# Kernel tuning notes

Hardware: AMD Instinct MI355X
Metric: run time of the kernel (lower is better)

The kernel has to match this reference:

```python
import jax, jax.numpy as jnp
import numpy as np

VOL_DIM = 256  # stored volume is [256,256,256,1]


def _deform(c, W1, b1, W2, b2, W3, b3, Wf, bf):
    # chain of 1x1x1 convs (== per-voxel matmuls) with cos activations, residual *5
    h = jnp.cos(jnp.einsum('...c,cd->...d', c, W1) + b1)
    h = jnp.cos(jnp.einsum('...c,cd->...d', h, W2) + b2)
    h = jnp.cos(jnp.einsum('...c,cd->...d', h, W3) + b3)
    return c + 5.0 * (jnp.einsum('...c,cd->...d', h, Wf) + bf)


def _trilinear_sample(vol, coords):
    # vol: [X,Y,Z,C]; coords: [...,3] in voxel units (identity nifti edges)
    X, Y, Z, _ = vol.shape
    hi = jnp.array([X - 1, Y - 1, Z - 1], dtype=coords.dtype)
    c = jnp.clip(coords, 0.0, hi)
    c0 = jnp.floor(c)
    f = c - c0
    i0 = c0.astype(jnp.int32)
    i1 = jnp.minimum(i0 + 1, jnp.array([X - 1, Y - 1, Z - 1], jnp.int32))
    x0, y0, z0 = i0[..., 0], i0[..., 1], i0[..., 2]
    x1, y1, z1 = i1[..., 0], i1[..., 1], i1[..., 2]
    fx, fy, fz = f[..., 0:1], f[..., 1:2], f[..., 2:3]
    gx, gy, gz = 1.0 - fx, 1.0 - fy, 1.0 - fz
    out = (vol[x0, y0, z0] * (gx * gy * gz) + vol[x1, y0, z0] * (fx * gy * gz)
         + vol[x0, y1, z0] * (gx * fy * gz) + vol[x0, y0, z1] * (gx * gy * fz)
         + vol[x1, y1, z0] * (fx * fy * gz) + vol[x1, y0, z1] * (fx * gy * fz)
         + vol[x0, y1, z1] * (gx * fy * fz) + vol[x1, y1, z1] * (fx * fy * fz))
    return out  # [...,C]


def setup_inputs() -> dict:
    key = jax.random.key(0)
    ks = jax.random.split(key, 12)
    B, P = 64, 32
    # coords in [0, 255] world==voxel units; extra intensity channel (unused by call)
    coords = jax.random.uniform(ks[0], (B, P, P, P, 3), jnp.float32) * (VOL_DIM - 1.0)
    inten = jax.random.normal(ks[1], (B, P, P, P, 1), jnp.float32)
    x = jnp.concatenate([coords, inten], axis=-1)
    s = 0.1
    return {
        'x': x,
        'W1': jax.random.normal(ks[2], (3, 32), jnp.float32) * s,
        'b1': jax.random.normal(ks[3], (32,), jnp.float32) * s,
        'W2': jax.random.normal(ks[4], (32, 32), jnp.float32) * s,
        'b2': jax.random.normal(ks[5], (32,), jnp.float32) * s,
        'W3': jax.random.normal(ks[6], (32, 32), jnp.float32) * s,
        'b3': jax.random.normal(ks[7], (32,), jnp.float32) * s,
        'Wf': jax.random.normal(ks[8], (32, 3), jnp.float32) * s,
        'bf': jax.random.normal(ks[9], (3,), jnp.float32) * s,
        'vol': jax.random.normal(ks[10], (VOL_DIM, VOL_DIM, VOL_DIM, 1), jnp.float32),
    }


def reference(x, W1, b1, W2, b2, W3, b3, Wf, bf, vol):
    c = x[..., 0:3]                                   # world coords
    c = _deform(c, W1, b1, W2, b2, W3, b3, Wf, bf)    # deformed coords
    return _trilinear_sample(vol, c)                  # [B,32,32,32,1]
```

## Files before the change

kernel.cpp:

```cpp
#include <hip/hip_runtime.h>


#define NPTS (64 * 32 * 32 * 32)
#define NBLK (NPTS / 256)
#define SSTR 40

#define BXN 86
#define BYN 128
#define BZN 86
#define NBRICK (BXN * BYN * BZN)
#define RETILE_T (NBRICK * 8)
#define RETILE_BLK (RETILE_T / 256)

typedef __attribute__((ext_vector_type(8))) short bf16x8;
typedef __attribute__((ext_vector_type(4))) short s16x4;
typedef __attribute__((ext_vector_type(4))) float f32x4;
typedef unsigned long long u64;
typedef unsigned short u16;

__device__ __forceinline__ short bf16rne(float f) {
    unsigned u = __builtin_bit_cast(unsigned, f);
    return (short)((u + 0x7fffu + ((u >> 16) & 1u)) >> 16);
}
__device__ __forceinline__ float bf16tof(short s) {
    return __builtin_bit_cast(float, ((unsigned)(unsigned short)s) << 16);
}
__device__ __forceinline__ float h2f(u16 h) {
    return (float)__builtin_bit_cast(_Float16, h);
}
__device__ __forceinline__ u16 f2h(float f) {
    return __builtin_bit_cast(u16, (_Float16)f);
}

__global__ __launch_bounds__(256)
void retile_k(const float4* __restrict__ vol, u64* __restrict__ dst) {
    int t   = blockIdx.x * 256 + threadIdx.x;
    int q   = t & 7;
    int gz  = (t >> 3) & 63;
    int gyx = t >> 9;
    int x = ((gyx >> 7) << 2) + (q >> 1);
    int y = ((gyx & 127) << 1) + (q & 1);
    float4 v = vol[(((x << 8) + y) << 6) + gz];
    u64 r =  (u64)f2h(v.x)
          | ((u64)f2h(v.y) << 16)
          | ((u64)f2h(v.z) << 32)
          | ((u64)f2h(v.w) << 48);
    dst[t] = r;
}

__global__ __launch_bounds__(256)
void retile_halo_k(const float* __restrict__ vol, u64* __restrict__ dst) {
    int t  = blockIdx.x * 256 + threadIdx.x;
    int q  = t & 7;
    int b  = t >> 3;
    int bz = (int)((unsigned)b % 86u);
    int r  = (int)((unsigned)b / 86u);
    int by = r & 127;
    int bx = r >> 7;
    int x  = min(bx * 3 + (q >> 1), 255);
    int y  = (by << 1) + (q & 1);
    int z0 = bz * 3;
    const float* row = vol + (((x << 8) + y) << 8);
    float v0 = row[z0];
    float v1 = row[min(z0 + 1, 255)];
    float v2 = row[min(z0 + 2, 255)];
    float v3 = row[min(z0 + 3, 255)];
    u64 rr = (u64)f2h(v0)
          | ((u64)f2h(v1) << 16)
          | ((u64)f2h(v2) << 32)
          | ((u64)f2h(v3) << 48);
    dst[t] = rr;
}

template <int MODE>
__global__ __launch_bounds__(256, 8)
void deform_sample_k(const float4* __restrict__ x,
                     const float4* __restrict__ W1,
                     const float4* __restrict__ b1,
                     const float*  __restrict__ W2,
                     const float*  __restrict__ b2,
                     const float*  __restrict__ W3,
                     const float*  __restrict__ b3,
                     const float*  __restrict__ Wf,
                     const float*  __restrict__ bf_,
                     const float*  __restrict__ volf,
                     const u64*    __restrict__ volh,
                     float* __restrict__ out)
{
    __shared__ short lds[4 * 64 * SSTR];
    const int tid  = threadIdx.x;
    const int lane = tid & 63;
    const int wv   = tid >> 6;
    const int m16  = lane & 15;
    const int q    = lane >> 4;
    short* __restrict__ L = &lds[wv * 64 * SSTR];

    const int p = blockIdx.x * 256 + tid;

    const float4 xv = x[p];
    const float c0 = xv.x, c1 = xv.y, c2 = xv.z;

    {
        bf16x8 hw;
        #pragma unroll
        for (int j4 = 0; j4 < 8; ++j4) {
            float4 wa = W1[j4], wb = W1[8 + j4], wc = W1[16 + j4], bb = b1[j4];
            float v0 = __cosf(fmaf(c0, wa.x, fmaf(c1, wb.x, fmaf(c2, wc.x, bb.x))));
            float v1 = __cosf(fmaf(c0, wa.y, fmaf(c1, wb.y, fmaf(c2, wc.y, bb.y))));
            float v2 = __cosf(fmaf(c0, wa.z, fmaf(c1, wb.z, fmaf(c2, wc.z, bb.z))));
            float v3 = __cosf(fmaf(c0, wa.w, fmaf(c1, wb.w, fmaf(c2, wc.w, bb.w))));
            int o = (j4 & 1) * 4;
            hw[o+0] = bf16rne(v0); hw[o+1] = bf16rne(v1);
            hw[o+2] = bf16rne(v2); hw[o+3] = bf16rne(v3);
            if (j4 & 1)
                *(bf16x8*)&L[lane * SSTR + (j4 - 1) * 4] = hw;
        }
    }
    __syncthreads();

    const float* const Wly[2] = { W2, W3 };
    const float* const bly[2] = { b2, b3 };
    #pragma unroll
    for (int ly = 0; ly < 2; ++ly) {
        const float* __restrict__ W  = Wly[ly];
        const float* __restrict__ bb = bly[ly];
        bf16x8 A0, A1;
        #pragma unroll
        for (int j = 0; j < 8; ++j) {
            A0[j] = bf16rne(W[(q * 8 + j) * 32 + m16]);
            A1[j] = bf16rne(W[(q * 8 + j) * 32 + 16 + m16]);
        }
        const float4 blo = *(const float4*)&bb[q * 4];
        const float4 bhi = *(const float4*)&bb[16 + q * 4];

        #pragma unroll
        for (int t = 0; t < 4; ++t) {
            bf16x8 bfrag = *(const bf16x8*)&L[(t * 16 + m16) * SSTR + q * 8];
            f32x4 z = { 0.f, 0.f, 0.f, 0.f };
            f32x4 d0 = __builtin_amdgcn_mfma_f32_16x16x32_bf16(A0, bfrag, z, 0, 0, 0);
            f32x4 d1 = __builtin_amdgcn_mfma_f32_16x16x32_bf16(A1, bfrag, z, 0, 0, 0);

            s16x4 w0, w1;
            w0[0] = bf16rne(__cosf(d0[0] + blo.x));
            w0[1] = bf16rne(__cosf(d0[1] + blo.y));
            w0[2] = bf16rne(__cosf(d0[2] + blo.z));
            w0[3] = bf16rne(__cosf(d0[3] + blo.w));
            w1[0] = bf16rne(__cosf(d1[0] + bhi.x));
            w1[1] = bf16rne(__cosf(d1[1] + bhi.y));
            w1[2] = bf16rne(__cosf(d1[2] + bhi.z));
            w1[3] = bf16rne(__cosf(d1[3] + bhi.w));
            *(s16x4*)&L[(t * 16 + m16) * SSTR + q * 4]      = w0;
            *(s16x4*)&L[(t * 16 + m16) * SSTR + 16 + q * 4] = w1;
        }
        __syncthreads();
    }

    float d0 = bf_[0], d1 = bf_[1], d2 = bf_[2];
    #pragma unroll
    for (int j4 = 0; j4 < 8; ++j4) {
        s16x4 v = *(const s16x4*)&L[lane * SSTR + j4 * 4];
        #pragma unroll
        for (int r = 0; r < 4; ++r) {
            float hv = bf16tof(v[r]);
            int ii = j4 * 4 + r;
            d0 = fmaf(hv, Wf[3*ii+0], d0);
            d1 = fmaf(hv, Wf[3*ii+1], d1);
            d2 = fmaf(hv, Wf[3*ii+2], d2);
        }
    }
    float e0 = fmaf(5.f, d0, c0);
    float e1 = fmaf(5.f, d1, c1);
    float e2 = fmaf(5.f, d2, c2);

    e0 = fminf(fmaxf(e0, 0.f), 255.f);
    e1 = fminf(fmaxf(e1, 0.f), 255.f);
    e2 = fminf(fmaxf(e2, 0.f), 255.f);
    float fl0 = floorf(e0), fl1 = floorf(e1), fl2 = floorf(e2);
    float fx = e0 - fl0, fy = e1 - fl1, fz = e2 - fl2;
    float gx = 1.f - fx, gy = 1.f - fy, gz = 1.f - fz;
    int x0 = (int)fl0, y0 = (int)fl1, z0 = (int)fl2;
    int x1 = min(x0 + 1, 255), y1 = min(y0 + 1, 255), z1 = min(z0 + 1, 255);

    float v000, v001, v010, v011, v100, v101, v110, v111;

    if constexpr (MODE == 2) {
        int bx = (int)((unsigned)x0 / 3u);  int lx = x0 - bx * 3;
        int by = y0 >> 1;                   int ly = y0 & 1;
        int bz = (int)((unsigned)z0 / 3u);  int lz = z0 - bz * 3;
        const char* vb = (const char*)volh;
        const int lineA = ((((bx << 7) + by) * 86) + bz) << 6;
        const int byB   = min(by + 1, 127);
        const int lineB = (ly == 0) ? lineA
                                    : (((((bx << 7) + byB) * 86) + bz) << 6);
        const int yrowB = (ly == 0) ? 1 : ((y0 == 255) ? 1 : 0);
        const int offA  = lx * 16 + ly * 8;
        const int offB  = lx * 16 + yrowB * 8;
        u64 LA0 = *(const u64*)(vb + lineA + offA);
        u64 LA1 = *(const u64*)(vb + lineA + offA + 16);
        u64 LB0 = *(const u64*)(vb + lineB + offB);
        u64 LB1 = *(const u64*)(vb + lineB + offB + 16);
        const int sh = lz * 16;
        u64 sA0 = LA0 >> sh, sA1 = LA1 >> sh, sB0 = LB0 >> sh, sB1 = LB1 >> sh;
        v000 = h2f((u16)sA0);  v001 = h2f((u16)(sA0 >> 16));
        v100 = h2f((u16)sA1);  v101 = h2f((u16)(sA1 >> 16));
        v010 = h2f((u16)sB0);  v011 = h2f((u16)(sB0 >> 16));
        v110 = h2f((u16)sB1);  v111 = h2f((u16)(sB1 >> 16));
    } else if constexpr (MODE == 1) {
        const int lz  = z0 & 3;
        const int zp  = (z0 >> 2) << 6;
        const int xp0 = ((x0 >> 2) << 19) | ((x0 & 3) << 4);
        const int xp1 = ((x1 >> 2) << 19) | ((x1 & 3) << 4);
        const int yp0 = ((y0 >> 1) << 12) | ((y0 & 1) << 3);
        const int yp1 = ((y1 >> 1) << 12) | ((y1 & 1) << 3);
        const char* vb = (const char*)volh;
        const int a00 = xp0 | yp0 | zp, a10 = xp1 | yp0 | zp;
        const int a01 = xp0 | yp1 | zp, a11 = xp1 | yp1 | zp;
        u64 L00 = *(const u64*)(vb + a00);
        u64 L10 = *(const u64*)(vb + a10);
        u64 L01 = *(const u64*)(vb + a01);
        u64 L11 = *(const u64*)(vb + a11);
        u64 H00 = 0, H10 = 0, H01 = 0, H11 = 0;
        const bool crossz = (lz == 3) && (z0 < 255);
        if (crossz) {
            H00 = *(const u64*)(vb + a00 + 64);
            H10 = *(const u64*)(vb + a10 + 64);
            H01 = *(const u64*)(vb + a01 + 64);
            H11 = *(const u64*)(vb + a11 + 64);
        }
        const int sh = lz * 16;
        const bool in_line = (lz < 3);
        auto ext = [&](u64 lo, u64 hi, float& a, float& b) {
            u64 s = lo >> sh;
            a = h2f((u16)s);
            float b_in = h2f((u16)(s >> 16));
            float b_nx = h2f((u16)hi);
            b = in_line ? b_in : (crossz ? b_nx : a);
        };
        ext(L00, H00, v000, v001);
        ext(L10, H10, v100, v101);
        ext(L01, H01, v010, v011);
        ext(L11, H11, v110, v111);
    } else {
        int b00 = (x0 << 16) | (y0 << 8);
        int b01 = (x0 << 16) | (y1 << 8);
        int b10 = (x1 << 16) | (y0 << 8);
        int b11 = (x1 << 16) | (y1 << 8);
        v000 = volf[b00 + z0]; v001 = volf[b00 + z1];
        v010 = volf[b01 + z0]; v011 = volf[b01 + z1];
        v100 = volf[b10 + z0]; v101 = volf[b10 + z1];
        v110 = volf[b11 + z0]; v111 = volf[b11 + z1];
    }

    float r = gz * (gy * (gx*v000 + fx*v100) + fy * (gx*v010 + fx*v110))
            + fz * (gy * (gx*v001 + fx*v101) + fy * (gx*v011 + fx*v111));

    out[p] = r;
}

extern "C" void kernel_launch(void* const* d_in, const int* in_sizes, int n_in,
                              void* d_out, int out_size, void* d_ws, size_t ws_size,
                              hipStream_t stream) {
    const float4* x   = (const float4*)d_in[0];
    const float4* W1  = (const float4*)d_in[1];
    const float4* b1  = (const float4*)d_in[2];
    const float*  W2  = (const float*)d_in[3];
    const float*  b2  = (const float*)d_in[4];
    const float*  W3  = (const float*)d_in[5];
    const float*  b3  = (const float*)d_in[6];
    const float*  Wf  = (const float*)d_in[7];
    const float*  bf_ = (const float*)d_in[8];
    const float*  vol = (const float*)d_in[9];
    float* out = (float*)d_out;

    const size_t needH = (size_t)NBRICK * 64;
    const size_t need1 = (size_t)4194304 * 8;
    if (ws_size >= needH) {
        u64* volh = (u64*)d_ws;
        retile_halo_k<<<RETILE_BLK, 256, 0, stream>>>(vol, volh);
        deform_sample_k<2><<<NBLK, 256, 0, stream>>>(x, W1, b1, W2, b2, W3, b3,
                                                     Wf, bf_, nullptr, volh, out);
    } else if (ws_size >= need1) {
        u64* volh = (u64*)d_ws;
        retile_k<<<16384, 256, 0, stream>>>((const float4*)vol, volh);
        deform_sample_k<1><<<NBLK, 256, 0, stream>>>(x, W1, b1, W2, b2, W3, b3,
                                                     Wf, bf_, nullptr, volh, out);
    } else {
        deform_sample_k<0><<<NBLK, 256, 0, stream>>>(x, W1, b1, W2, b2, W3, b3,
                                                     Wf, bf_, vol, nullptr, out);
    }
}
```

Before: 213.4 us.

## Add full y-halo fp16 brick layout so each sample reads one contiguous line

Adds a new retile kernel that builds one brick per y row with a y+1 halo (3 x-slices by 2 y-rows by 4 z), doubling the staged volume footprint, plus a new sampling mode that fetches all 8 corners as four consecutive u64 loads from a single 64-byte brick. The goal is to remove the second-line fetch and the branchy offset logic of the previous halo layout, which loaded from two bricks when y was odd. In exchange the retile writes about twice as many bytes and needs a larger workspace; if the workspace is too small the code falls back to the old path.

```diff
diff --git a/kernel.cpp b/kernel.cpp
--- a/kernel.cpp
+++ b/kernel.cpp
@@ -11,10 +11,17 @@
 #define NBRICK (BXN * BYN * BZN)
 #define RETILE_T (NBRICK * 8)
 #define RETILE_BLK (RETILE_T / 256)
+#define HALO_BYTES ((size_t)NBRICK * 64)
+
+#define NBRICK_F (86 * 256 * 86)
+#define RETILE2_T (NBRICK_F * 4)
+#define RETILE2_BLK (RETILE2_T / 256)
+#define FULL_BYTES ((size_t)NBRICK_F * 64)
 
 typedef __attribute__((ext_vector_type(8))) short bf16x8;
 typedef __attribute__((ext_vector_type(4))) short s16x4;
 typedef __attribute__((ext_vector_type(4))) float f32x4;
+typedef __attribute__((ext_vector_type(2))) unsigned long long u64x2;
 typedef unsigned long long u64;
 typedef unsigned short u16;
 
@@ -72,6 +79,36 @@
     dst[t] = rr;
 }
 
+__global__ __launch_bounds__(256)
+void retile_full2_k(const float* __restrict__ vol, u64* __restrict__ dst) {
+    int t  = blockIdx.x * 256 + threadIdx.x;
+    int dx = t & 3;
+    int b  = t >> 2;
+    int bz = (int)((unsigned)b % 86u);
+    int r  = (int)((unsigned)b / 86u);
+    int by = r & 255;
+    int bx = r >> 8;
+    int x  = min(bx * 3 + dx, 255);
+    int y1 = min(by + 1, 255);
+    int z0 = bz * 3;
+    int zl = (z0 > 252) ? 252 : z0;
+    const float* row0 = vol + (((x << 8) + by) << 8) + zl;
+    const float* row1 = vol + (((x << 8) + y1) << 8) + zl;
+    float va[4], vb[4];
+    __builtin_memcpy(va, row0, 16);
+    __builtin_memcpy(vb, row1, 16);
+    if (z0 == 255) {
+        va[0] = va[1] = va[2] = va[3];
+        vb[0] = vb[1] = vb[2] = vb[3];
+    }
+    u64 lo = (u64)f2h(va[0]) | ((u64)f2h(va[1]) << 16)
+           | ((u64)f2h(va[2]) << 32) | ((u64)f2h(va[3]) << 48);
+    u64 hi = (u64)f2h(vb[0]) | ((u64)f2h(vb[1]) << 16)
+           | ((u64)f2h(vb[2]) << 32) | ((u64)f2h(vb[3]) << 48);
+    u64x2 st; st.x = lo; st.y = hi;
+    *(u64x2*)(dst + (b << 3) + (dx << 1)) = st;
+}
+
 template <int MODE>
 __global__ __launch_bounds__(256, 8)
 void deform_sample_k(const float4* __restrict__ x,
@@ -183,7 +220,21 @@
 
     float v000, v001, v010, v011, v100, v101, v110, v111;
 
-    if constexpr (MODE == 2) {
+    if constexpr (MODE == 3) {
+        int bx = (int)((unsigned)x0 / 3u);  int lx = x0 - bx * 3;
+        int bz = (int)((unsigned)z0 / 3u);  int lz = z0 - bz * 3;
+        const u64* g = volh + ((((bx << 8) + y0) * 86 + bz) << 3) + (lx << 1);
+        u64 g0 = g[0];
+        u64 g1 = g[1];
+        u64 g2 = g[2];
+        u64 g3 = g[3];
+        const int sh = lz * 16;
+        u64 s0 = g0 >> sh, s1 = g1 >> sh, s2 = g2 >> sh, s3 = g3 >> sh;
+        v000 = h2f((u16)s0);  v001 = h2f((u16)(s0 >> 16));
+        v010 = h2f((u16)s1);  v011 = h2f((u16)(s1 >> 16));
+        v100 = h2f((u16)s2);  v101 = h2f((u16)(s2 >> 16));
+        v110 = h2f((u16)s3);  v111 = h2f((u16)(s3 >> 16));
+    } else if constexpr (MODE == 2) {
         int bx = (int)((unsigned)x0 / 3u);  int lx = x0 - bx * 3;
         int by = y0 >> 1;                   int ly = y0 & 1;
         int bz = (int)((unsigned)z0 / 3u);  int lz = z0 - bz * 3;
@@ -272,9 +323,16 @@
     const float*  vol = (const float*)d_in[9];
     float* out = (float*)d_out;
 
-    const size_t needH = (size_t)NBRICK * 64;
+    const size_t needF = FULL_BYTES;
+    const size_t needH = HALO_BYTES;
     const size_t need1 = (size_t)4194304 * 8;
-    if (ws_size >= needH) {
+
+    if (ws_size >= needF) {
+        u64* volh = (u64*)d_ws;
+        retile_full2_k<<<RETILE2_BLK, 256, 0, stream>>>(vol, volh);
+        deform_sample_k<3><<<NBLK, 256, 0, stream>>>(x, W1, b1, W2, b2, W3, b3,
+                                                     Wf, bf_, nullptr, volh, out);
+    } else if (ws_size >= needH) {
         u64* volh = (u64*)d_ws;
         retile_halo_k<<<RETILE_BLK, 256, 0, stream>>>(vol, volh);
         deform_sample_k<2><<<NBLK, 256, 0, stream>>>(x, W1, b1, W2, b2, W3, b3,
```

Measured after the change: 211.2 us. No clear change (-1.0%).
